# Kernel optimization log

Measured on AMD Instinct MI355X. Metric: run time of the kernel, lower is better.

The kernel has to match this reference:

```python
import jax, jax.numpy as jnp
import numpy as np

G = 4          # moe_groups
EPG = 4        # experts per group = e_num // moe_groups
E = 16         # e_num
KG = 2         # moe_max_groups
K = 2          # moe_max_k
GTP = 0.9      # moe_group_top_p
TP = 0.9       # moe_top_p
SCALE = 1.0 / float(np.sqrt(G))  # group_scale


def setup_inputs() -> dict:
    key = jax.random.key(0)
    ks = jax.random.split(key, 6)
    B, T, D, H = 2, 1024, 512, 2048  # H = 4*emb_dim per SwiGLU_FFN(emb_dim, 4*emb_dim)
    x = jax.random.normal(ks[0], (B, T, D), jnp.float32)
    Wr = jax.random.normal(ks[1], (D, G), jnp.float32) * 0.02      # group_router weight
    br = jnp.zeros((G,), jnp.float32)                               # group_router bias
    Wgate = jax.random.normal(ks[2], (G, D, EPG), jnp.float32) * 0.02  # per-group gates
    bgate = jnp.zeros((G, EPG), jnp.float32)
    W1 = jax.random.normal(ks[3], (E, D, H), jnp.float32) * 0.02   # SwiGLU gate proj
    W3 = jax.random.normal(ks[4], (E, D, H), jnp.float32) * 0.02   # SwiGLU up proj
    W2 = jax.random.normal(ks[5], (E, H, D), jnp.float32) * 0.02   # SwiGLU down proj
    return {"x": x, "Wr": Wr, "br": br, "Wgate": Wgate, "bgate": bgate,
            "W1": W1, "W3": W3, "W2": W2}


def _routing_weights(xf, Wr, br, Wgate, bgate):
    # Returns combined per-(token, expert) weight (N, E): group_renorm * expert_renorm * SCALE.
    N = xf.shape[0]
    # ---- group-level top-p routing ----
    gp = jax.nn.softmax(xf @ Wr + br, axis=-1)                      # (N, G)
    order = jnp.argsort(-gp, axis=-1)
    sp_k = jnp.take_along_axis(gp, order, axis=-1)[:, :KG]          # top-KG probs, descending
    idx_k = order[:, :KG]
    act = jnp.cumsum(sp_k, axis=-1) <= GTP
    act = act.at[:, 0].set(True)                                    # always keep best group
    mp = sp_k * act
    rn = mp / (jnp.sum(mp, axis=-1, keepdims=True) + 1e-9)
    w_group = jnp.zeros((N, G), xf.dtype).at[jnp.arange(N)[:, None], idx_k].set(rn)
    # ---- expert-level top-p routing within each group ----
    ep = jax.nn.softmax(jnp.einsum('nd,gde->nge', xf, Wgate) + bgate, axis=-1)  # (N, G, EPG)
    eorder = jnp.argsort(-ep, axis=-1)
    esp = jnp.take_along_axis(ep, eorder, axis=-1)[:, :, :K]
    eidx = eorder[:, :, :K]
    eact = jnp.cumsum(esp, axis=-1) <= TP
    eact = eact.at[:, :, 0].set(True)                               # always keep best expert
    emp = esp * eact
    ern = emp / (jnp.sum(emp, axis=-1, keepdims=True) + 1e-9)
    w_exp = jnp.zeros((N, G, EPG), xf.dtype).at[
        jnp.arange(N)[:, None, None], jnp.arange(G)[None, :, None], eidx].set(ern)
    return (w_group[:, :, None] * w_exp * SCALE).reshape(N, E)      # (N, E)


def reference(x, Wr, br, Wgate, bgate, W1, W3, W2):
    B, T, D = x.shape
    xf = x.reshape(-1, D)                                           # (N, D)
    tw = _routing_weights(xf, Wr, br, Wgate, bgate)                 # (N, E)
    out = jnp.zeros_like(xf)
    for e in range(E):  # fixed structural loop over experts
        h = jax.nn.silu(xf @ W1[e]) * (xf @ W3[e])                  # SwiGLU hidden (N, H)
        out = out + tw[:, e:e + 1] * (h @ W2[e])
    return out.reshape(B, T, D)
```

## Files before the change

### kernel.cpp

```cpp
#include <hip/hip_runtime.h>
#include <math.h>

typedef unsigned short u16;
typedef unsigned int   u32;
typedef short s16x8 __attribute__((ext_vector_type(8)));
typedef float f32x4 __attribute__((ext_vector_type(4)));

#define N_TOK 2048
#define DIM   512
#define HID   2048
#define NE    16
#define NG    4
#define EPG   4
#define MAXT  2048

#define BM 64
#define BN 128
#define BK 64

#define WS_CNT    0
#define WS_OFF    128
#define WS_TOKIDX 256
#define WS_TW     (WS_TOKIDX + NE*MAXT*4)
#define WS_XB     (WS_TW + N_TOK*NE*4)
#define WS_HBUF   (WS_XB + (size_t)N_TOK*DIM*2)
#define WS_W1T    (WS_HBUF + (size_t)8192*HID*2)
#define WS_W3T    (WS_W1T + (size_t)NE*HID*DIM*2)
#define WS_W2T    (WS_W3T + (size_t)NE*HID*DIM*2)
#define WS_SLOT   (WS_W2T + (size_t)NE*DIM*HID*2)
#define WS_BUF2   WS_W1T

__device__ __forceinline__ int* ws_i32(void* ws, size_t off) { return (int*)((char*)ws + off); }

__device__ __forceinline__ u16 f2b(float f) {
    union { float f; u32 i; } v; v.f = f;
    u32 b = v.i;
    u32 r = b + 0x7FFFu + ((b >> 16) & 1u);
    return (u16)(r >> 16);
}

__device__ __forceinline__ void gl_lds16(const u16* g, u16* l) {
    __builtin_amdgcn_global_load_lds((const __attribute__((address_space(1))) void*)g,
                                     (__attribute__((address_space(3))) void*)l, 16, 0, 0);
}

__global__ __launch_bounds__(1024) void prep_kernel(
    const float* __restrict__ x, const float* __restrict__ Wr, const float* __restrict__ br,
    const float* __restrict__ Wgate, const float* __restrict__ bgate,
    const float* __restrict__ W1, const float* __restrict__ W3, void* ws)
{
    __shared__ u16 T[2][128*128];
    int tid = threadIdx.x;
    int bid = blockIdx.x;

    if (bid < 128) {
        int t = bid * 16 + (tid >> 6);
        int lane = tid & 63;

        float xl[8];
        {
            const float4* xr = (const float4*)(x + (size_t)t*DIM + lane*8);
            float4 a = xr[0], b = xr[1];
            xl[0]=a.x; xl[1]=a.y; xl[2]=a.z; xl[3]=a.w;
            xl[4]=b.x; xl[5]=b.y; xl[6]=b.z; xl[7]=b.w;
        }
        {
            union { u16 h[8]; uint4 q; } pk;
            #pragma unroll
            for (int i = 0; i < 8; i++) pk.h[i] = f2b(xl[i]);
            u16* xb = (u16*)((char*)ws + WS_XB);
            *(uint4*)(xb + (size_t)t*DIM + lane*8) = pk.q;
        }

        float gl[NG] = {0.f,0.f,0.f,0.f};
        float el[NE];
        #pragma unroll
        for (int e = 0; e < NE; e++) el[e] = 0.f;

        {
            const float4* Wr4 = (const float4*)Wr;
            #pragma unroll
            for (int c = 0; c < 8; c++) {
                float4 w = Wr4[lane*8 + c];
                gl[0] += xl[c]*w.x; gl[1] += xl[c]*w.y;
                gl[2] += xl[c]*w.z; gl[3] += xl[c]*w.w;
            }
        }
        {
            const float4* Wg4 = (const float4*)Wgate;
            #pragma unroll
            for (int g = 0; g < NG; g++) {
                #pragma unroll
                for (int c = 0; c < 8; c++) {
                    float4 w = Wg4[(size_t)g*DIM + lane*8 + c];
                    el[g*4+0] += xl[c]*w.x; el[g*4+1] += xl[c]*w.y;
                    el[g*4+2] += xl[c]*w.z; el[g*4+3] += xl[c]*w.w;
                }
            }
        }

        #pragma unroll
        for (int g = 0; g < NG; g++)
            #pragma unroll
            for (int s = 32; s; s >>= 1) gl[g] += __shfl_xor(gl[g], s);
        #pragma unroll
        for (int e = 0; e < NE; e++)
            #pragma unroll
            for (int s = 32; s; s >>= 1) el[e] += __shfl_xor(el[e], s);

        if (lane != 0) return;

        float gp[NG];
        float mx = -1e30f;
        #pragma unroll
        for (int g = 0; g < NG; g++) { gl[g] += br[g]; mx = fmaxf(mx, gl[g]); }
        float sum = 0.f;
        #pragma unroll
        for (int g = 0; g < NG; g++) { gp[g] = expf(gl[g] - mx); sum += gp[g]; }
        #pragma unroll
        for (int g = 0; g < NG; g++) gp[g] /= sum;

        int i0 = 0;
        #pragma unroll
        for (int g = 1; g < NG; g++) if (gp[g] > gp[i0]) i0 = g;
        int i1 = -1;
        #pragma unroll
        for (int g = 0; g < NG; g++) { if (g == i0) continue; if (i1 < 0 || gp[g] > gp[i1]) i1 = g; }

        bool act1 = (gp[i0] + gp[i1]) <= 0.9f;
        float mp0 = gp[i0], mp1 = act1 ? gp[i1] : 0.f;
        float inv = 1.f / (mp0 + mp1 + 1e-9f);
        float wg[NG] = {0.f,0.f,0.f,0.f};
        wg[i0] = mp0 * inv;
        wg[i1] = mp1 * inv;

        float tw[NE];
        #pragma unroll
        for (int g = 0; g < NG; g++) {
            float ep[EPG];
            float emx = -1e30f;
            #pragma unroll
            for (int j = 0; j < EPG; j++) {
                float v = el[g*4 + j] + bgate[g*4 + j];
                ep[j] = v; emx = fmaxf(emx, v);
            }
            float es = 0.f;
            #pragma unroll
            for (int j = 0; j < EPG; j++) { ep[j] = expf(ep[j] - emx); es += ep[j]; }
            #pragma unroll
            for (int j = 0; j < EPG; j++) ep[j] /= es;

            int j0 = 0;
            #pragma unroll
            for (int j = 1; j < EPG; j++) if (ep[j] > ep[j0]) j0 = j;
            int j1 = -1;
            #pragma unroll
            for (int j = 0; j < EPG; j++) { if (j == j0) continue; if (j1 < 0 || ep[j] > ep[j1]) j1 = j; }

            bool ea1 = (ep[j0] + ep[j1]) <= 0.9f;
            float e0 = ep[j0], e1 = ea1 ? ep[j1] : 0.f;
            float einv = 1.f / (e0 + e1 + 1e-9f);
            float we[EPG] = {0.f,0.f,0.f,0.f};
            we[j0] = e0 * einv;
            we[j1] = e1 * einv;
            #pragma unroll
            for (int j = 0; j < EPG; j++) tw[g*4 + j] = wg[g] * we[j] * 0.5f;
        }

        float* twT = (float*)((char*)ws + WS_TW);
        #pragma unroll
        for (int e = 0; e < NE; e++) twT[(size_t)e*N_TOK + t] = tw[e];
        return;
    }

    int bx = bid - 128;
    int j = tid & 31, i0 = tid >> 5;
    int tg0 = bx * 4;

    const float* src; u16* dst; int k0, n0;
    float4 v0, v1, v2, v3;

    auto setup = [&](int tg) {
        int mat = tg >> 10, e = (tg >> 6) & 15, w = tg & 63;
        const float* s  = mat ? W3 : W1;
        u16* d = (u16*)((char*)ws + (mat ? WS_W3T : WS_W1T));
        k0 = (w & 3) << 7; n0 = (w >> 2) << 7;
        src = s + (size_t)e*DIM*HID + (size_t)(k0 + 4*i0)*HID + n0 + 4*j;
        dst = d + (size_t)e*HID*DIM;
    };
    auto issue_loads = [&]() {
        v0 = *(const float4*)(src);
        v1 = *(const float4*)(src + HID);
        v2 = *(const float4*)(src + 2*HID);
        v3 = *(const float4*)(src + 3*HID);
    };

    setup(tg0);
    issue_loads();

    for (int it = 0; it < 4; ++it) {
        u16* dstc = dst; int k0c = k0, n0c = n0;
        u16* Tb = &T[it & 1][0];

        int pc = 4 * (i0 ^ ((j & 15) << 1));
        union { u16 h[4]; uint2 q; } p;
        p.h[0]=f2b(v0.x); p.h[1]=f2b(v1.x); p.h[2]=f2b(v2.x); p.h[3]=f2b(v3.x);
        *(uint2*)(&Tb[(4*j+0)*128 + pc]) = p.q;
        p.h[0]=f2b(v0.y); p.h[1]=f2b(v1.y); p.h[2]=f2b(v2.y); p.h[3]=f2b(v3.y);
        *(uint2*)(&Tb[(4*j+1)*128 + pc]) = p.q;
        p.h[0]=f2b(v0.z); p.h[1]=f2b(v1.z); p.h[2]=f2b(v2.z); p.h[3]=f2b(v3.z);
        *(uint2*)(&Tb[(4*j+2)*128 + pc]) = p.q;
        p.h[0]=f2b(v0.w); p.h[1]=f2b(v1.w); p.h[2]=f2b(v2.w); p.h[3]=f2b(v3.w);
        *(uint2*)(&Tb[(4*j+3)*128 + pc]) = p.q;

        if (it + 1 < 4) { setup(tg0 + it + 1); issue_loads(); }

        asm volatile("s_waitcnt lgkmcnt(0)" ::: "memory");
        __builtin_amdgcn_s_barrier();

        #pragma unroll
        for (int ph = 0; ph < 2; ++ph) {
            int idx = tid + ph*1024;
            int nr = idx >> 4, sg = idx & 15;
            int cp = (2*sg) ^ (((nr >> 2) & 15) << 1);
            *(s16x8*)(dstc + (size_t)(n0c+nr)*DIM + k0c + sg*8) = *(const s16x8*)(&Tb[nr*128 + 4*cp]);
        }
    }
}

__global__ __launch_bounds__(1024) void expert_scan_kernel(void* ws)
{
    int tid = threadIdx.x;
    int e = tid >> 6, lane = tid & 63;
    const float* twT = (const float*)((char*)ws + WS_TW) + (size_t)e*N_TOK;
    int* tok = ws_i32(ws, WS_TOKIDX) + e*MAXT;
    __shared__ int scnt[NE];
    __shared__ int soff[NE+1];

    float v[32];
    #pragma unroll
    for (int r = 0; r < 32; r++) v[r] = twT[r*64 + lane];

    unsigned long long lanemask = (1ull << lane) - 1ull;
    int base = 0;
    #pragma unroll
    for (int r = 0; r < 32; r++) {
        bool a = v[r] > 0.f;
        unsigned long long m = __ballot(a);
        if (a) tok[base + __popcll(m & lanemask)] = r*64 + lane;
        base += __popcll(m);
    }
    if (lane == 0) scnt[e] = base;
    __syncthreads();
    if (tid == 0) {
        int* cnt = ws_i32(ws, WS_CNT);
        int* off = ws_i32(ws, WS_OFF);
        int s = 0;
        for (int i = 0; i < NE; i++) { cnt[i] = scnt[i]; off[i] = s; soff[i] = s; s += scnt[i]; }
        off[NE] = s; soff[NE] = s;
    }
    __syncthreads();

    int* slot_of = ws_i32(ws, WS_SLOT) + e*N_TOK;
    int base2 = soff[e];
    #pragma unroll
    for (int r = 0; r < 32; r++) {
        bool a = v[r] > 0.f;
        unsigned long long m = __ballot(a);
        int pre = __popcll(m & lanemask);
        slot_of[r*64 + lane] = a ? (base2 + pre) : -1;
        base2 += __popcll(m);
    }
}

__global__ __launch_bounds__(256) void gemm1_fast(const float* __restrict__ W2, void* ws)
{
    __shared__ __align__(16) u16 SM[20480];
    int z = blockIdx.z;
    int tid = threadIdx.x;

    if (z == NE) {
        u16* T2 = SM;
        u16* W2T = (u16*)((char*)ws + WS_W2T);
        int slot = blockIdx.x + 16*blockIdx.y;
        int j = tid & 31, i = tid >> 5;
        #pragma unroll 1
        for (int tt = 0; tt < 2; ++tt) {
            int tile = slot + tt*512;
            int e = tile >> 6, w = tile & 63;
            int k0 = (w & 15) << 7, n0 = (w >> 4) << 7;
            const float* s = W2 + (size_t)e*HID*DIM + (size_t)k0*DIM + n0 + 4*j;
            if (tt) __syncthreads();
            #pragma unroll
            for (int c = 0; c < 4; ++c) {
                int kb = 4*i + 32*c;
                const float* base = s + (size_t)kb*DIM;
                float4 v0 = *(const float4*)(base);
                float4 v1 = *(const float4*)(base + DIM);
                float4 v2 = *(const float4*)(base + 2*DIM);
                float4 v3 = *(const float4*)(base + 3*DIM);
                int pc = 4 * ((i + 8*c) ^ ((j & 15) << 1));
                union { u16 h[4]; uint2 q; } p;
                p.h[0]=f2b(v0.x); p.h[1]=f2b(v1.x); p.h[2]=f2b(v2.x); p.h[3]=f2b(v3.x);
                *(uint2*)(&T2[(4*j+0)*128 + pc]) = p.q;
                p.h[0]=f2b(v0.y); p.h[1]=f2b(v1.y); p.h[2]=f2b(v2.y); p.h[3]=f2b(v3.y);
                *(uint2*)(&T2[(4*j+1)*128 + pc]) = p.q;
                p.h[0]=f2b(v0.z); p.h[1]=f2b(v1.z); p.h[2]=f2b(v2.z); p.h[3]=f2b(v3.z);
                *(uint2*)(&T2[(4*j+2)*128 + pc]) = p.q;
                p.h[0]=f2b(v0.w); p.h[1]=f2b(v1.w); p.h[2]=f2b(v2.w); p.h[3]=f2b(v3.w);
                *(uint2*)(&T2[(4*j+3)*128 + pc]) = p.q;
            }
            __syncthreads();
            u16* d = W2T + (size_t)e*DIM*HID;
            #pragma unroll
            for (int ph = 0; ph < 8; ++ph) {
                int idx = tid + ph*256;
                int nr = idx >> 4, sg = idx & 15;
                int cp = (2*sg) ^ (((nr >> 2) & 15) << 1);
                *(s16x8*)(d + (size_t)(n0+nr)*HID + k0 + sg*8) = *(const s16x8*)(&T2[nr*128 + 4*cp]);
            }
        }
        return;
    }

    int e  = z;
    const int* cnt = ws_i32(ws, WS_CNT);
    int ce = cnt[e];
    int m0 = blockIdx.y * BM;
    if (m0 >= ce) return;
    int n0 = blockIdx.x * BN;

    const int* off = ws_i32(ws, WS_OFF);
    const int* tok = ws_i32(ws, WS_TOKIDX) + e*MAXT;
    const u16* xb  = (const u16*)((char*)ws + WS_XB);
    const u16* W1T = (const u16*)((char*)ws + WS_W1T) + (size_t)e*HID*DIM;
    const u16* W3T = (const u16*)((char*)ws + WS_W3T) + (size_t)e*HID*DIM;
    u16* hbuf = (u16*)((char*)ws + WS_HBUF);
    int obase = off[e] + m0;

    u16* As  = SM;
    u16* Bs0 = SM + 4096;
    u16* Bs1 = SM + 12288;

    int wave = tid >> 6, lane = tid & 63;
    int quad = lane >> 4, l16 = lane & 15;
    int swz  = l16 & 7;
    int r8 = lane >> 3, sg = lane & 7;
    int swk = ((sg ^ r8) << 3);

    int m_a0 = m0 + wave*16 + r8;     if (m_a0 >= ce) m_a0 = ce - 1;
    int m_a1 = m0 + wave*16 + 8 + r8; if (m_a1 >= ce) m_a1 = ce - 1;
    const u16* arow0 = xb + (size_t)tok[m_a0]*DIM + swk;
    const u16* arow1 = xb + (size_t)tok[m_a1]*DIM + swk;
    const u16* b1row[4]; const u16* b3row[4];
    #pragma unroll
    for (int i = 0; i < 4; i++) {
        size_t nr = (size_t)(n0 + wave*32 + i*8 + r8)*DIM + swk;
        b1row[i] = W1T + nr;
        b3row[i] = W3T + nr;
    }

    f32x4 acc1[4][2], acc3[4][2];
    #pragma unroll
    for (int mt = 0; mt < 4; mt++)
        #pragma unroll
        for (int nt = 0; nt < 2; nt++) {
            acc1[mt][nt] = (f32x4){0.f,0.f,0.f,0.f};
            acc3[mt][nt] = (f32x4){0.f,0.f,0.f,0.f};
        }

    for (int k0 = 0; k0 < DIM; k0 += BK) {
        gl_lds16(arow0 + k0, &As[(wave*16)*BK]);
        gl_lds16(arow1 + k0, &As[(wave*16 + 8)*BK]);
        #pragma unroll
        for (int i = 0; i < 4; i++) {
            gl_lds16(b1row[i] + k0, &Bs0[(wave*32 + i*8)*BK]);
            gl_lds16(b3row[i] + k0, &Bs1[(wave*32 + i*8)*BK]);
        }
        __syncthreads();

        #pragma unroll
        for (int kk = 0; kk < BK; kk += 32) {
            int jj = (kk >> 3) + quad;
            int so = ((jj ^ swz) << 3);
            s16x8 af[4];
            #pragma unroll
            for (int mt = 0; mt < 4; mt++)
                af[mt] = *(const s16x8*)(&As[(mt*16 + l16)*BK + so]);
            #pragma unroll
            for (int nt = 0; nt < 2; nt++) {
                int n = wave*32 + nt*16 + l16;
                s16x8 b1 = *(const s16x8*)(&Bs0[n*BK + so]);
                s16x8 b3 = *(const s16x8*)(&Bs1[n*BK + so]);
                #pragma unroll
                for (int mt = 0; mt < 4; mt++) {
                    acc1[mt][nt] = __builtin_amdgcn_mfma_f32_16x16x32_bf16(af[mt], b1, acc1[mt][nt], 0, 0, 0);
                    acc3[mt][nt] = __builtin_amdgcn_mfma_f32_16x16x32_bf16(af[mt], b3, acc3[mt][nt], 0, 0, 0);
                }
            }
        }
        __syncthreads();
    }

    #pragma unroll
    for (int mt = 0; mt < 4; mt++) {
        #pragma unroll
        for (int r = 0; r < 4; r++) {
            int row = mt*16 + quad*4 + r;
            if (m0 + row < ce) {
                #pragma unroll
                for (int nt = 0; nt < 2; nt++) {
                    float a = acc1[mt][nt][r];
                    float b = acc3[mt][nt][r];
                    float h = (a / (1.f + expf(-a))) * b;
                    int col = wave*32 + nt*16 + l16;
                    hbuf[(size_t)(obase + row)*HID + n0 + col] = f2b(h);
                }
            }
        }
    }
}

__global__ __launch_bounds__(256) void gemm2_fast(void* ws)
{
    int e  = blockIdx.z;
    const int* cnt = ws_i32(ws, WS_CNT);
    int ce = cnt[e];
    int m0 = blockIdx.y * BM;
    if (m0 >= ce) return;
    int n0 = blockIdx.x * BN;

    const int* off = ws_i32(ws, WS_OFF);
    const int* tok = ws_i32(ws, WS_TOKIDX) + e*MAXT;
    const float* twT = (const float*)((char*)ws + WS_TW);
    const u16* hbuf = (const u16*)((char*)ws + WS_HBUF);
    const u16* W2T = (const u16*)((char*)ws + WS_W2T) + (size_t)e*DIM*HID;
    float* buf2 = (float*)((char*)ws + WS_BUF2);
    int abase = off[e] + m0;
    int total = off[NE];

    __shared__ u16 As[BM*BK];
    __shared__ u16 Bs[BN*BK];

    int tid = threadIdx.x;
    int wave = tid >> 6, lane = tid & 63;
    int quad = lane >> 4, l16 = lane & 15;
    int swz  = l16 & 7;
    int r8 = lane >> 3, sg = lane & 7;
    int swk = ((sg ^ r8) << 3);

    int ar0 = abase + wave*16 + r8;      if (ar0 > total - 1) ar0 = total - 1;
    int ar1 = abase + wave*16 + 8 + r8;  if (ar1 > total - 1) ar1 = total - 1;
    const u16* arow0 = hbuf + (size_t)ar0*HID + swk;
    const u16* arow1 = hbuf + (size_t)ar1*HID + swk;
    const u16* brow[4];
    #pragma unroll
    for (int i = 0; i < 4; i++)
        brow[i] = W2T + (size_t)(n0 + wave*32 + i*8 + r8)*HID + swk;

    f32x4 acc[4][2];
    #pragma unroll
    for (int mt = 0; mt < 4; mt++)
        #pragma unroll
        for (int nt = 0; nt < 2; nt++) acc[mt][nt] = (f32x4){0.f,0.f,0.f,0.f};

    for (int k0 = 0; k0 < HID; k0 += BK) {
        gl_lds16(arow0 + k0, &As[(wave*16)*BK]);
        gl_lds16(arow1 + k0, &As[(wave*16 + 8)*BK]);
        #pragma unroll
        for (int i = 0; i < 4; i++)
            gl_lds16(brow[i] + k0, &Bs[(wave*32 + i*8)*BK]);
        __syncthreads();

        #pragma unroll
        for (int kk = 0; kk < BK; kk += 32) {
            int jj = (kk >> 3) + quad;
            int so = ((jj ^ swz) << 3);
            s16x8 af[4];
            #pragma unroll
            for (int mt = 0; mt < 4; mt++)
                af[mt] = *(const s16x8*)(&As[(mt*16 + l16)*BK + so]);
            #pragma unroll
            for (int nt = 0; nt < 2; nt++) {
                int n = wave*32 + nt*16 + l16;
                s16x8 bfr = *(const s16x8*)(&Bs[n*BK + so]);
                #pragma unroll
                for (int mt = 0; mt < 4; mt++)
                    acc[mt][nt] = __builtin_amdgcn_mfma_f32_16x16x32_bf16(af[mt], bfr, acc[mt][nt], 0, 0, 0);
            }
        }
        __syncthreads();
    }

    #pragma unroll
    for (int mt = 0; mt < 4; mt++) {
        #pragma unroll
        for (int r = 0; r < 4; r++) {
            int row = mt*16 + quad*4 + r;
            if (m0 + row < ce) {
                int t = tok[m0 + row];
                float s = twT[(size_t)e*N_TOK + t];
                #pragma unroll
                for (int nt = 0; nt < 2; nt++) {
                    int col = wave*32 + nt*16 + l16;
                    buf2[(size_t)(abase + row)*DIM + n0 + col] = acc[mt][nt][r] * s;
                }
            }
        }
    }
}

__global__ __launch_bounds__(128) void gather_kernel(void* ws, float* __restrict__ out)
{
    int t = blockIdx.x;
    int tid = threadIdx.x;
    const int* slot_of = ws_i32(ws, WS_SLOT);
    const float* buf2 = (const float*)((char*)ws + WS_BUF2);

    int d = tid * 4;
    float4 acc = {0.f, 0.f, 0.f, 0.f};
    #pragma unroll
    for (int e = 0; e < NE; e++) {
        int s = slot_of[e*N_TOK + t];
        if (s >= 0) {
            float4 v = *(const float4*)(buf2 + (size_t)s*DIM + d);
            acc.x += v.x; acc.y += v.y; acc.z += v.z; acc.w += v.w;
        }
    }
    *(float4*)(out + (size_t)t*DIM + d) = acc;
}

extern "C" void kernel_launch(void* const* d_in, const int* in_sizes, int n_in,
                              void* d_out, int out_size, void* d_ws, size_t ws_size,
                              hipStream_t stream)
{
    const float* x     = (const float*)d_in[0];
    const float* Wr    = (const float*)d_in[1];
    const float* br    = (const float*)d_in[2];
    const float* Wgate = (const float*)d_in[3];
    const float* bgate = (const float*)d_in[4];
    const float* W1    = (const float*)d_in[5];
    const float* W3    = (const float*)d_in[6];
    const float* W2    = (const float*)d_in[7];
    float* out = (float*)d_out;

    prep_kernel<<<640, 1024, 0, stream>>>(x, Wr, br, Wgate, bgate, W1, W3, d_ws);
    expert_scan_kernel<<<1, 1024, 0, stream>>>(d_ws);
    gemm1_fast<<<dim3(HID/BN, N_TOK/BM, NE + 1), 256, 0, stream>>>(W2, d_ws);
    gemm2_fast<<<dim3(DIM/BN, N_TOK/BM, NE), 256, 0, stream>>>(d_ws);
    gather_kernel<<<N_TOK, 128, 0, stream>>>(d_ws, out);
}
```

Baseline: 336.7 us.

## Double-buffer LDS in both expert GEMMs to overlap global loads with MFMA

Both expert GEMM kernels now use two LDS buffers. Each iteration issues the async global-to-LDS loads for the next K tile, then waits with a partial vmcnt so only the current tile's loads must be complete before computing on it. This hides global load latency behind MFMA work instead of stalling at a full barrier every tile. The cost is double the shared memory (80KB in gemm1, 48KB in gemm2), which may lower occupancy. It also relies on hand-counted vmcnt values that must match the number of outstanding load instructions.

Result: faster. 326.2 us (-3.1%).

```diff
diff --git a/kernel.cpp b/kernel.cpp
--- a/kernel.cpp
+++ b/kernel.cpp
@@ -275,7 +275,7 @@
 
 __global__ __launch_bounds__(256) void gemm1_fast(const float* __restrict__ W2, void* ws)
 {
-    __shared__ __align__(16) u16 SM[20480];
+    __shared__ __align__(16) u16 SM[40960];
     int z = blockIdx.z;
     int tid = threadIdx.x;
 
@@ -338,10 +338,6 @@
     u16* hbuf = (u16*)((char*)ws + WS_HBUF);
     int obase = off[e] + m0;
 
-    u16* As  = SM;
-    u16* Bs0 = SM + 4096;
-    u16* Bs1 = SM + 12288;
-
     int wave = tid >> 6, lane = tid & 63;
     int quad = lane >> 4, l16 = lane & 15;
     int swz  = l16 & 7;
@@ -369,16 +365,22 @@
             acc3[mt][nt] = (f32x4){0.f,0.f,0.f,0.f};
         }
 
-    for (int k0 = 0; k0 < DIM; k0 += BK) {
-        gl_lds16(arow0 + k0, &As[(wave*16)*BK]);
-        gl_lds16(arow1 + k0, &As[(wave*16 + 8)*BK]);
+    auto stage = [&](int b, int k0) {
+        u16* As_  = SM + b*20480;
+        u16* Bs0_ = As_ + 4096;
+        u16* Bs1_ = As_ + 12288;
+        gl_lds16(arow0 + k0, &As_[(wave*16)*BK]);
+        gl_lds16(arow1 + k0, &As_[(wave*16 + 8)*BK]);
         #pragma unroll
         for (int i = 0; i < 4; i++) {
-            gl_lds16(b1row[i] + k0, &Bs0[(wave*32 + i*8)*BK]);
-            gl_lds16(b3row[i] + k0, &Bs1[(wave*32 + i*8)*BK]);
-        }
-        __syncthreads();
-
+            gl_lds16(b1row[i] + k0, &Bs0_[(wave*32 + i*8)*BK]);
+            gl_lds16(b3row[i] + k0, &Bs1_[(wave*32 + i*8)*BK]);
+        }
+    };
+    auto compute = [&](int b) {
+        u16* As_  = SM + b*20480;
+        u16* Bs0_ = As_ + 4096;
+        u16* Bs1_ = As_ + 12288;
         #pragma unroll
         for (int kk = 0; kk < BK; kk += 32) {
             int jj = (kk >> 3) + quad;
@@ -386,12 +388,12 @@
             s16x8 af[4];
             #pragma unroll
             for (int mt = 0; mt < 4; mt++)
-                af[mt] = *(const s16x8*)(&As[(mt*16 + l16)*BK + so]);
+                af[mt] = *(const s16x8*)(&As_[(mt*16 + l16)*BK + so]);
             #pragma unroll
             for (int nt = 0; nt < 2; nt++) {
                 int n = wave*32 + nt*16 + l16;
-                s16x8 b1 = *(const s16x8*)(&Bs0[n*BK + so]);
-                s16x8 b3 = *(const s16x8*)(&Bs1[n*BK + so]);
+                s16x8 b1 = *(const s16x8*)(&Bs0_[n*BK + so]);
+                s16x8 b3 = *(const s16x8*)(&Bs1_[n*BK + so]);
                 #pragma unroll
                 for (int mt = 0; mt < 4; mt++) {
                     acc1[mt][nt] = __builtin_amdgcn_mfma_f32_16x16x32_bf16(af[mt], b1, acc1[mt][nt], 0, 0, 0);
@@ -399,8 +401,24 @@
                 }
             }
         }
-        __syncthreads();
-    }
+    };
+
+    stage(0, 0);
+    #pragma unroll 1
+    for (int kt = 0; kt < 7; ++kt) {
+        int cur = kt & 1;
+        stage(cur ^ 1, (kt + 1)*BK);
+        asm volatile("s_waitcnt vmcnt(10)" ::: "memory");
+        __builtin_amdgcn_s_barrier();
+        asm volatile("" ::: "memory");
+        compute(cur);
+        __builtin_amdgcn_s_barrier();
+        asm volatile("" ::: "memory");
+    }
+    asm volatile("s_waitcnt vmcnt(0)" ::: "memory");
+    __builtin_amdgcn_s_barrier();
+    asm volatile("" ::: "memory");
+    compute(1);
 
     #pragma unroll
     for (int mt = 0; mt < 4; mt++) {
@@ -423,6 +441,7 @@
 
 __global__ __launch_bounds__(256) void gemm2_fast(void* ws)
 {
+    __shared__ __align__(16) u16 SM[24576];
     int e  = blockIdx.z;
     const int* cnt = ws_i32(ws, WS_CNT);
     int ce = cnt[e];
@@ -439,9 +458,6 @@
     int abase = off[e] + m0;
     int total = off[NE];
 
-    __shared__ u16 As[BM*BK];
-    __shared__ u16 Bs[BN*BK];
-
     int tid = threadIdx.x;
     int wave = tid >> 6, lane = tid & 63;
     int quad = lane >> 4, l16 = lane & 15;
@@ -464,14 +480,18 @@
         #pragma unroll
         for (int nt = 0; nt < 2; nt++) acc[mt][nt] = (f32x4){0.f,0.f,0.f,0.f};
 
-    for (int k0 = 0; k0 < HID; k0 += BK) {
-        gl_lds16(arow0 + k0, &As[(wave*16)*BK]);
-        gl_lds16(arow1 + k0, &As[(wave*16 + 8)*BK]);
+    auto stage = [&](int b, int k0) {
+        u16* As_ = SM + b*12288;
+        u16* Bs_ = As_ + 4096;
+        gl_lds16(arow0 + k0, &As_[(wave*16)*BK]);
+        gl_lds16(arow1 + k0, &As_[(wave*16 + 8)*BK]);
         #pragma unroll
         for (int i = 0; i < 4; i++)
-            gl_lds16(brow[i] + k0, &Bs[(wave*32 + i*8)*BK]);
-        __syncthreads();
-
+            gl_lds16(brow[i] + k0, &Bs_[(wave*32 + i*8)*BK]);
+    };
+    auto compute = [&](int b) {
+        u16* As_ = SM + b*12288;
+        u16* Bs_ = As_ + 4096;
         #pragma unroll
         for (int kk = 0; kk < BK; kk += 32) {
             int jj = (kk >> 3) + quad;
@@ -479,18 +499,34 @@
             s16x8 af[4];
             #pragma unroll
             for (int mt = 0; mt < 4; mt++)
-                af[mt] = *(const s16x8*)(&As[(mt*16 + l16)*BK + so]);
+                af[mt] = *(const s16x8*)(&As_[(mt*16 + l16)*BK + so]);
             #pragma unroll
             for (int nt = 0; nt < 2; nt++) {
                 int n = wave*32 + nt*16 + l16;
-                s16x8 bfr = *(const s16x8*)(&Bs[n*BK + so]);
+                s16x8 bfr = *(const s16x8*)(&Bs_[n*BK + so]);
                 #pragma unroll
                 for (int mt = 0; mt < 4; mt++)
                     acc[mt][nt] = __builtin_amdgcn_mfma_f32_16x16x32_bf16(af[mt], bfr, acc[mt][nt], 0, 0, 0);
             }
         }
-        __syncthreads();
-    }
+    };
+
+    stage(0, 0);
+    #pragma unroll 1
+    for (int kt = 0; kt < 31; ++kt) {
+        int cur = kt & 1;
+        stage(cur ^ 1, (kt + 1)*BK);
+        asm volatile("s_waitcnt vmcnt(6)" ::: "memory");
+        __builtin_amdgcn_s_barrier();
+        asm volatile("" ::: "memory");
+        compute(cur);
+        __builtin_amdgcn_s_barrier();
+        asm volatile("" ::: "memory");
+    }
+    asm volatile("s_waitcnt vmcnt(0)" ::: "memory");
+    __builtin_amdgcn_s_barrier();
+    asm volatile("" ::: "memory");
+    compute(1);
 
     #pragma unroll
     for (int mt = 0; mt < 4; mt++) {
```

## Double-buffer LDS tiles in expert GEMMs to overlap global loads with MFMA

Applied to the files above, without the earlier changes.

Both expert GEMM kernels now use two LDS buffers. The next K-tile's global-to-LDS loads are issued before computing the current tile, and partial vmcnt waits plus raw s_barrier replace the full __syncthreads pairs. This is meant to hide global memory latency behind MFMA work. It doubles LDS use per block (80KB for gemm1), which may reduce occupancy, and it relies on vmcnt counting the exact number of outstanding loads.

After: 323.3 us. 4.0% less time.

```diff
diff --git a/kernel.cpp b/kernel.cpp
--- a/kernel.cpp
+++ b/kernel.cpp
@@ -275,7 +275,7 @@
 
 __global__ __launch_bounds__(256) void gemm1_fast(const float* __restrict__ W2, void* ws)
 {
-    __shared__ __align__(16) u16 SM[20480];
+    __shared__ __align__(16) u16 SM[40960];
     int z = blockIdx.z;
     int tid = threadIdx.x;
 
@@ -338,10 +338,6 @@
     u16* hbuf = (u16*)((char*)ws + WS_HBUF);
     int obase = off[e] + m0;
 
-    u16* As  = SM;
-    u16* Bs0 = SM + 4096;
-    u16* Bs1 = SM + 12288;
-
     int wave = tid >> 6, lane = tid & 63;
     int quad = lane >> 4, l16 = lane & 15;
     int swz  = l16 & 7;
@@ -369,16 +365,16 @@
             acc3[mt][nt] = (f32x4){0.f,0.f,0.f,0.f};
         }
 
-    for (int k0 = 0; k0 < DIM; k0 += BK) {
-        gl_lds16(arow0 + k0, &As[(wave*16)*BK]);
-        gl_lds16(arow1 + k0, &As[(wave*16 + 8)*BK]);
+    auto stage = [&](u16* B, int k0) {
+        gl_lds16(arow0 + k0, B + (wave*16)*BK);
+        gl_lds16(arow1 + k0, B + (wave*16 + 8)*BK);
         #pragma unroll
         for (int i = 0; i < 4; i++) {
-            gl_lds16(b1row[i] + k0, &Bs0[(wave*32 + i*8)*BK]);
-            gl_lds16(b3row[i] + k0, &Bs1[(wave*32 + i*8)*BK]);
-        }
-        __syncthreads();
-
+            gl_lds16(b1row[i] + k0, B + 4096 + (wave*32 + i*8)*BK);
+            gl_lds16(b3row[i] + k0, B + 12288 + (wave*32 + i*8)*BK);
+        }
+    };
+    auto compute = [&](const u16* B) {
         #pragma unroll
         for (int kk = 0; kk < BK; kk += 32) {
             int jj = (kk >> 3) + quad;
@@ -386,12 +382,12 @@
             s16x8 af[4];
             #pragma unroll
             for (int mt = 0; mt < 4; mt++)
-                af[mt] = *(const s16x8*)(&As[(mt*16 + l16)*BK + so]);
+                af[mt] = *(const s16x8*)(B + (mt*16 + l16)*BK + so);
             #pragma unroll
             for (int nt = 0; nt < 2; nt++) {
                 int n = wave*32 + nt*16 + l16;
-                s16x8 b1 = *(const s16x8*)(&Bs0[n*BK + so]);
-                s16x8 b3 = *(const s16x8*)(&Bs1[n*BK + so]);
+                s16x8 b1 = *(const s16x8*)(B + 4096 + n*BK + so);
+                s16x8 b3 = *(const s16x8*)(B + 12288 + n*BK + so);
                 #pragma unroll
                 for (int mt = 0; mt < 4; mt++) {
                     acc1[mt][nt] = __builtin_amdgcn_mfma_f32_16x16x32_bf16(af[mt], b1, acc1[mt][nt], 0, 0, 0);
@@ -399,8 +395,34 @@
                 }
             }
         }
-        __syncthreads();
-    }
+    };
+
+    u16* SM0 = SM;
+    u16* SM1 = SM + 20480;
+
+    stage(SM0, 0);
+    #pragma unroll 1
+    for (int kt2 = 0; kt2 < 3; ++kt2) {
+        int kb = kt2*2*BK;
+        stage(SM1, kb + BK);
+        asm volatile("s_waitcnt vmcnt(10)" ::: "memory");
+        __builtin_amdgcn_s_barrier();
+        compute(SM0);
+        __builtin_amdgcn_s_barrier();
+        stage(SM0, kb + 2*BK);
+        asm volatile("s_waitcnt vmcnt(10)" ::: "memory");
+        __builtin_amdgcn_s_barrier();
+        compute(SM1);
+        __builtin_amdgcn_s_barrier();
+    }
+    stage(SM1, 7*BK);
+    asm volatile("s_waitcnt vmcnt(10)" ::: "memory");
+    __builtin_amdgcn_s_barrier();
+    compute(SM0);
+    __builtin_amdgcn_s_barrier();
+    asm volatile("s_waitcnt vmcnt(0)" ::: "memory");
+    __builtin_amdgcn_s_barrier();
+    compute(SM1);
 
     #pragma unroll
     for (int mt = 0; mt < 4; mt++) {
@@ -423,6 +445,7 @@
 
 __global__ __launch_bounds__(256) void gemm2_fast(void* ws)
 {
+    __shared__ __align__(16) u16 SM[24576];
     int e  = blockIdx.z;
     const int* cnt = ws_i32(ws, WS_CNT);
     int ce = cnt[e];
@@ -439,9 +462,6 @@
     int abase = off[e] + m0;
     int total = off[NE];
 
-    __shared__ u16 As[BM*BK];
-    __shared__ u16 Bs[BN*BK];
-
     int tid = threadIdx.x;
     int wave = tid >> 6, lane = tid & 63;
     int quad = lane >> 4, l16 = lane & 15;
@@ -464,14 +484,14 @@
         #pragma unroll
         for (int nt = 0; nt < 2; nt++) acc[mt][nt] = (f32x4){0.f,0.f,0.f,0.f};
 
-    for (int k0 = 0; k0 < HID; k0 += BK) {
-        gl_lds16(arow0 + k0, &As[(wave*16)*BK]);
-        gl_lds16(arow1 + k0, &As[(wave*16 + 8)*BK]);
+    auto stage = [&](u16* B, int k0) {
+        gl_lds16(arow0 + k0, B + (wave*16)*BK);
+        gl_lds16(arow1 + k0, B + (wave*16 + 8)*BK);
         #pragma unroll
         for (int i = 0; i < 4; i++)
-            gl_lds16(brow[i] + k0, &Bs[(wave*32 + i*8)*BK]);
-        __syncthreads();
-
+            gl_lds16(brow[i] + k0, B + 4096 + (wave*32 + i*8)*BK);
+    };
+    auto compute = [&](const u16* B) {
         #pragma unroll
         for (int kk = 0; kk < BK; kk += 32) {
             int jj = (kk >> 3) + quad;
@@ -479,18 +499,44 @@
             s16x8 af[4];
             #pragma unroll
             for (int mt = 0; mt < 4; mt++)
-                af[mt] = *(const s16x8*)(&As[(mt*16 + l16)*BK + so]);
+                af[mt] = *(const s16x8*)(B + (mt*16 + l16)*BK + so);
             #pragma unroll
             for (int nt = 0; nt < 2; nt++) {
                 int n = wave*32 + nt*16 + l16;
-                s16x8 bfr = *(const s16x8*)(&Bs[n*BK + so]);
+                s16x8 bfr = *(const s16x8*)(B + 4096 + n*BK + so);
                 #pragma unroll
                 for (int mt = 0; mt < 4; mt++)
                     acc[mt][nt] = __builtin_amdgcn_mfma_f32_16x16x32_bf16(af[mt], bfr, acc[mt][nt], 0, 0, 0);
             }
         }
-        __syncthreads();
-    }
+    };
+
+    u16* SM0 = SM;
+    u16* SM1 = SM + 12288;
+
+    stage(SM0, 0);
+    #pragma unroll 1
+    for (int kt2 = 0; kt2 < 15; ++kt2) {
+        int kb = kt2*2*BK;
+        stage(SM1, kb + BK);
+        asm volatile("s_waitcnt vmcnt(6)" ::: "memory");
+        __builtin_amdgcn_s_barrier();
+        compute(SM0);
+        __builtin_amdgcn_s_barrier();
+        stage(SM0, kb + 2*BK);
+        asm volatile("s_waitcnt vmcnt(6)" ::: "memory");
+        __builtin_amdgcn_s_barrier();
+        compute(SM1);
+        __builtin_amdgcn_s_barrier();
+    }
+    stage(SM1, 31*BK);
+    asm volatile("s_waitcnt vmcnt(6)" ::: "memory");
+    __builtin_amdgcn_s_barrier();
+    compute(SM0);
+    __builtin_amdgcn_s_barrier();
+    asm volatile("s_waitcnt vmcnt(0)" ::: "memory");
+    __builtin_amdgcn_s_barrier();
+    compute(SM1);
 
     #pragma unroll
     for (int mt = 0; mt < 4; mt++) {
```
